# Kernel optimization log

Hardware: AMD Instinct MI355X
Metric: run time of the kernel (lower is better)

The kernel has to match this reference:

```python
import jax, jax.numpy as jnp
import numpy as np

V, D, L, H, S, MLP = 50257, 1024, 4, 16, 2048, 4
HD = D // H
EPS = 1e-5


def setup_inputs() -> dict:
    key = jax.random.key(0)
    ks = jax.random.split(key, 16)
    s = 0.02
    inp = {
        "input_ids": jax.random.randint(ks[0], (1, S), 0, V, dtype=jnp.int64),
        "emb": jax.random.normal(ks[1], (V, D), jnp.float32) * s,
        "Wq": jax.random.normal(ks[2], (L, D, D), jnp.float32) * s,
        "Wk": jax.random.normal(ks[3], (L, D, D), jnp.float32) * s,
        "Wv": jax.random.normal(ks[4], (L, D, D), jnp.float32) * s,
        "Wo": jax.random.normal(ks[5], (L, D, D), jnp.float32) * s,
        "ln1_g": jnp.ones((L, D), jnp.float32),
        "ln1_b": jnp.zeros((L, D), jnp.float32),
        "ln2_g": jnp.ones((L, D), jnp.float32),
        "ln2_b": jnp.zeros((L, D), jnp.float32),
        "W1": jax.random.normal(ks[6], (L, D, MLP * D), jnp.float32) * s,
        "b1": jnp.zeros((L, MLP * D), jnp.float32),
        "W2": jax.random.normal(ks[7], (L, MLP * D, D), jnp.float32) * s,
        "b2": jnp.zeros((L, D), jnp.float32),
        "lnf_g": jnp.ones((D,), jnp.float32),
        "lnf_b": jnp.zeros((D,), jnp.float32),
    }
    return inp


def _layer_norm(x, g, b):
    m = jnp.mean(x, axis=-1, keepdims=True)
    v = jnp.mean(jnp.square(x - m), axis=-1, keepdims=True)
    return (x - m) * jax.lax.rsqrt(v + EPS) * g + b


def _rope_cos_sin(seq_len, dtype):
    # standard RoPE: inv_freq over pairs, rotate-half convention
    inv_freq = 1.0 / (10000.0 ** (jnp.arange(0, HD, 2, dtype=jnp.float32) / HD))
    ang = jnp.arange(seq_len, dtype=jnp.float32)[:, None] * inv_freq[None, :]  # [S, HD/2]
    ang = jnp.concatenate([ang, ang], axis=-1)  # [S, HD]
    return jnp.cos(ang).astype(dtype), jnp.sin(ang).astype(dtype)


def _rotate_half(x):
    x1, x2 = x[..., : HD // 2], x[..., HD // 2 :]
    return jnp.concatenate([-x2, x1], axis=-1)


def _gpt_forward(input_ids, emb, Wq, Wk, Wv, Wo, ln1_g, ln1_b, ln2_g, ln2_b, W1, b1, W2, b2, lnf_g, lnf_b):
    B, T = input_ids.shape
    x = emb[input_ids]  # [B, T, D]
    cos, sin = _rope_cos_sin(T, x.dtype)  # [T, HD]
    cos, sin = cos[None, None], sin[None, None]  # broadcast to [B, H, T, HD]
    mask = jnp.triu(jnp.ones((T, T), dtype=bool), k=1)
    scale = 1.0 / np.sqrt(HD)
    for l in range(L):
        h = _layer_norm(x, ln1_g[l], ln1_b[l])
        q = (h @ Wq[l]).reshape(B, T, H, HD).transpose(0, 2, 1, 3)
        k = (h @ Wk[l]).reshape(B, T, H, HD).transpose(0, 2, 1, 3)
        v = (h @ Wv[l]).reshape(B, T, H, HD).transpose(0, 2, 1, 3)
        q = q * cos + _rotate_half(q) * sin
        k = k * cos + _rotate_half(k) * sin
        scores = jnp.einsum("bhsd,bhtd->bhst", q, k) * scale  # full [B,H,T,T]
        scores = jnp.where(mask, -jnp.inf, scores)
        attn = jax.nn.softmax(scores, axis=-1)
        out = jnp.einsum("bhst,bhtd->bhsd", attn, v)
        out = out.transpose(0, 2, 1, 3).reshape(B, T, D) @ Wo[l]
        x = x + out
        h = _layer_norm(x, ln2_g[l], ln2_b[l])
        x = x + (jax.nn.gelu(h @ W1[l] + b1[l], approximate=False) @ W2[l] + b2[l])
    x = _layer_norm(x, lnf_g, lnf_b)
    logits = x @ emb.T  # tied lm_head
    return logits


def reference(input_ids, emb, Wq, Wk, Wv, Wo, ln1_g, ln1_b, ln2_g, ln2_b, W1, b1, W2, b2, lnf_g, lnf_b):
    return _gpt_forward(input_ids, emb, Wq, Wk, Wv, Wo, ln1_g, ln1_b, ln2_g, ln2_b, W1, b1, W2, b2, lnf_g, lnf_b)
```

## Files before the change

kernel.cpp:

```cpp
#include <hip/hip_runtime.h>
#include <hip/hip_bf16.h>
#include <math.h>

#define TT   2048
#define DD   1024
#define NL   4
#define NH   16
#define HDIM 64
#define VV   50257
#define DMLP 4096

typedef __bf16 bf16_t;
typedef __bf16 bf16x8 __attribute__((ext_vector_type(8)));
typedef __bf16 bf16x4 __attribute__((ext_vector_type(4)));
typedef float  f32x4  __attribute__((ext_vector_type(4)));

__device__ inline float block_reduce_sum(float v) {
    __shared__ float sbuf[4];
#pragma unroll
    for (int o = 32; o > 0; o >>= 1) v += __shfl_down(v, o, 64);
    int w = threadIdx.x >> 6, lane = threadIdx.x & 63;
    __syncthreads();
    if (lane == 0) sbuf[w] = v;
    __syncthreads();
    return sbuf[0] + sbuf[1] + sbuf[2] + sbuf[3];
}

__device__ inline float block_reduce_max(float v) {
    __shared__ float mbuf[4];
#pragma unroll
    for (int o = 32; o > 0; o >>= 1) v = fmaxf(v, __shfl_down(v, o, 64));
    int w = threadIdx.x >> 6, lane = threadIdx.x & 63;
    __syncthreads();
    if (lane == 0) mbuf[w] = v;
    __syncthreads();
    return fmaxf(fmaxf(mbuf[0], mbuf[1]), fmaxf(mbuf[2], mbuf[3]));
}

__device__ __forceinline__ void async16(const bf16_t* g, bf16_t* l) {
    __builtin_amdgcn_global_load_lds(
        (const __attribute__((address_space(1))) unsigned int*)g,
        (__attribute__((address_space(3))) unsigned int*)l,
        16, 0, 0);
}

__global__ void trans_w_kernel(const float* __restrict__ in, bf16_t* __restrict__ out,
                               int K, int N, long inStride, long outStride) {
    __shared__ float tile[32][33];
    long zin  = (long)blockIdx.z * inStride;
    long zout = (long)blockIdx.z * outStride;
    int tx = threadIdx.x, ty = threadIdx.y;
    int n = blockIdx.x * 32 + tx;
    int k0 = blockIdx.y * 32;
#pragma unroll
    for (int i = 0; i < 4; i++)
        tile[ty + i * 8][tx] = in[zin + (long)(k0 + ty + i * 8) * N + n];
    __syncthreads();
    int k = k0 + tx;
#pragma unroll
    for (int i = 0; i < 4; i++) {
        int nn = blockIdx.x * 32 + ty + i * 8;
        out[zout + (long)nn * K + k] = (bf16_t)tile[tx][ty + i * 8];
    }
}

__global__ void cvt_kernel(const float* __restrict__ in, bf16_t* __restrict__ out, long n4) {
    long i = (long)blockIdx.x * 256 + threadIdx.x;
    if (i >= n4) return;
    float4 v = *(const float4*)(in + i * 4);
    bf16x4 o;
    o[0] = (bf16_t)v.x; o[1] = (bf16_t)v.y; o[2] = (bf16_t)v.z; o[3] = (bf16_t)v.w;
    *(bf16x4*)(out + i * 4) = o;
}

__global__ void gather_kernel(const int* __restrict__ ids, const float* __restrict__ emb,
                              float* __restrict__ x) {
    int row = blockIdx.x;
    int id = ids[row];
    const float4* src = (const float4*)(emb + (long)id * DD);
    float4* dst = (float4*)(x + (long)row * DD);
    dst[threadIdx.x] = src[threadIdx.x];
}

__global__ __launch_bounds__(256) void ln_kernel(const float* __restrict__ x,
                                                 const float* __restrict__ g,
                                                 const float* __restrict__ b,
                                                 bf16_t* __restrict__ out) {
    int row = blockIdx.x, tid = threadIdx.x;
    float4 v = *(const float4*)(x + (long)row * DD + tid * 4);
    float s = v.x + v.y + v.z + v.w;
    s = block_reduce_sum(s);
    float mean = s * (1.0f / DD);
    float dx = v.x - mean, dy = v.y - mean, dz = v.z - mean, dw = v.w - mean;
    float sq = dx * dx + dy * dy + dz * dz + dw * dw;
    sq = block_reduce_sum(sq);
    float inv = rsqrtf(sq * (1.0f / DD) + 1e-5f);
    float4 gv = *(const float4*)(g + tid * 4);
    float4 bv = *(const float4*)(b + tid * 4);
    bf16x4 o;
    o[0] = (bf16_t)(dx * inv * gv.x + bv.x);
    o[1] = (bf16_t)(dy * inv * gv.y + bv.y);
    o[2] = (bf16_t)(dz * inv * gv.z + bv.z);
    o[3] = (bf16_t)(dw * inv * gv.w + bv.w);
    *(bf16x4*)(out + (long)row * DD + tid * 4) = o;
}

__global__ void rope_kernel(bf16_t* __restrict__ qkv) {
    int t = blockIdx.x;
    int pIdx = blockIdx.y * 256 + threadIdx.x;
    int h = pIdx >> 5, i = pIdx & 31;
    float invf = powf(10000.0f, -(float)i * (1.0f / 32.0f));
    float ang = (float)t * invf;
    float s, c;
    sincosf(ang, &s, &c);
    long base = (long)t * 3072 + h * 64 + i;
    float q1 = (float)qkv[base], q2 = (float)qkv[base + 32];
    qkv[base]      = (bf16_t)((q1 * c - q2 * s) * 0.125f);
    qkv[base + 32] = (bf16_t)((q2 * c + q1 * s) * 0.125f);
    float k1 = (float)qkv[base + 1024], k2 = (float)qkv[base + 1056];
    qkv[base + 1024] = (bf16_t)(k1 * c - k2 * s);
    qkv[base + 1056] = (bf16_t)(k2 * c + k1 * s);
}

__global__ void trans_v_kernel(const bf16_t* __restrict__ qkv, bf16_t* __restrict__ vT) {
    __shared__ bf16_t tile[32][33];
    int t0 = blockIdx.x * 32, d0 = blockIdx.y * 32;
    int tx = threadIdx.x, ty = threadIdx.y;
#pragma unroll
    for (int i = 0; i < 4; i++)
        tile[ty + i * 8][tx] = qkv[(long)(t0 + ty + i * 8) * 3072 + 2048 + d0 + tx];
    __syncthreads();
    int t = t0 + tx;
#pragma unroll
    for (int i = 0; i < 4; i++) {
        int d = d0 + ty + i * 8;
        vT[(long)d * TT + t] = tile[tx][ty + i * 8];
    }
}

__global__ __launch_bounds__(256) void softmax_kernel(bf16_t* __restrict__ S) {
    int i = blockIdx.x, h = blockIdx.y, tid = threadIdx.x;
    bf16_t* row = S + ((long)h * TT + i) * TT;
    int len = i + 1;
    float e[8];
    float mx = -1e30f;
#pragma unroll
    for (int jj = 0; jj < 8; jj++) {
        int j = tid + jj * 256;
        e[jj] = (j < len) ? (float)row[j] : -1e30f;
        mx = fmaxf(mx, e[jj]);
    }
    mx = block_reduce_max(mx);
    float sum = 0.0f;
#pragma unroll
    for (int jj = 0; jj < 8; jj++) {
        int j = tid + jj * 256;
        if (j < len) { e[jj] = __expf(e[jj] - mx); sum += e[jj]; } else e[jj] = 0.0f;
    }
    sum = block_reduce_sum(sum);
    float inv = 1.0f / sum;
#pragma unroll
    for (int jj = 0; jj < 8; jj++)
        row[tid + jj * 256] = (bf16_t)(e[jj] * inv);
}

template <int OBF, int BIAS, int GELU, int RES>
__global__ __launch_bounds__(256, 2) void gemm_bt(
    const bf16_t* __restrict__ A, long sA, int lda,
    const bf16_t* __restrict__ Bt, long sB, int ldb,
    void* __restrict__ Cv, long sC, int ldc,
    const float* __restrict__ bias, const float* res,
    int M, int N, int K) {
    __shared__ bf16_t lA[128 * 32];
    __shared__ bf16_t lB[128 * 32];
    int bz = blockIdx.z;
    A += (long)bz * sA;
    Bt += (long)bz * sB;
    long cOff = (long)bz * sC;
    int m0 = blockIdx.x * 128, n0 = blockIdx.y * 128;
    int t = threadIdx.x;
    int wave = t >> 6, lane = t & 63;
    int wm = wave >> 1, wn = wave & 1;
    int lr = lane & 15, lq = lane >> 4;
    f32x4 acc[4][4];
#pragma unroll
    for (int a = 0; a < 4; a++)
#pragma unroll
        for (int b = 0; b < 4; b++) acc[a][b] = (f32x4){0.f, 0.f, 0.f, 0.f};

    int rowHalf = wave * 16 + (lane >> 2);
    int seg8 = (lane & 3) * 8;
    int rA0 = m0 + rowHalf;       if (rA0 > M - 1) rA0 = M - 1;
    int rA1 = m0 + rowHalf + 64;  if (rA1 > M - 1) rA1 = M - 1;
    int rB0 = n0 + rowHalf;       if (rB0 > N - 1) rB0 = N - 1;
    int rB1 = n0 + rowHalf + 64;  if (rB1 > N - 1) rB1 = N - 1;
    const bf16_t* gA0 = A + (long)rA0 * lda + seg8;
    const bf16_t* gA1 = A + (long)rA1 * lda + seg8;
    const bf16_t* gB0 = Bt + (long)rB0 * ldb + seg8;
    const bf16_t* gB1 = Bt + (long)rB1 * ldb + seg8;
    bf16_t* dA0 = lA + wave * 512;
    bf16_t* dA1 = lA + 2048 + wave * 512;
    bf16_t* dB0 = lB + wave * 512;
    bf16_t* dB1 = lB + 2048 + wave * 512;

    for (int k0 = 0; k0 < K; k0 += 32) {
        __syncthreads();
        async16(gA0 + k0, dA0);
        async16(gA1 + k0, dA1);
        async16(gB0 + k0, dB0);
        async16(gB1 + k0, dB1);
        __syncthreads();
        bf16x8 af[4], bfr[4];
#pragma unroll
        for (int mt = 0; mt < 4; mt++)
            af[mt] = *(const bf16x8*)&lA[(wm * 64 + mt * 16 + lr) * 32 + lq * 8];
#pragma unroll
        for (int nt = 0; nt < 4; nt++)
            bfr[nt] = *(const bf16x8*)&lB[(wn * 64 + nt * 16 + lr) * 32 + lq * 8];
#pragma unroll
        for (int mt = 0; mt < 4; mt++)
#pragma unroll
            for (int nt = 0; nt < 4; nt++)
                acc[mt][nt] = __builtin_amdgcn_mfma_f32_16x16x32_bf16(af[mt], bfr[nt], acc[mt][nt], 0, 0, 0);
    }
#pragma unroll
    for (int nt = 0; nt < 4; nt++) {
        int col = n0 + wn * 64 + nt * 16 + lr;
        if (col >= N) continue;
        float bb = BIAS ? bias[col] : 0.0f;
#pragma unroll
        for (int mt = 0; mt < 4; mt++) {
            int rbase = m0 + wm * 64 + mt * 16 + lq * 4;
#pragma unroll
            for (int r = 0; r < 4; r++) {
                int rowi = rbase + r;
                if (rowi >= M) continue;
                float val = acc[mt][nt][r] + bb;
                if (GELU) val = 0.5f * val * (1.0f + erff(val * 0.70710678118f));
                if (RES) val += res[(long)rowi * ldc + col];
                long idx = cOff + (long)rowi * ldc + col;
                if (OBF) ((bf16_t*)Cv)[idx] = (bf16_t)val;
                else     ((float*)Cv)[idx] = val;
            }
        }
    }
}

extern "C" void kernel_launch(void* const* d_in, const int* in_sizes, int n_in,
                              void* d_out, int out_size, void* d_ws, size_t ws_size,
                              hipStream_t stream) {
    (void)in_sizes; (void)n_in; (void)out_size; (void)ws_size;
    const int*   ids  = (const int*)d_in[0];
    const float* emb  = (const float*)d_in[1];
    const float* Wq   = (const float*)d_in[2];
    const float* Wk   = (const float*)d_in[3];
    const float* Wv   = (const float*)d_in[4];
    const float* Wo   = (const float*)d_in[5];
    const float* ln1g = (const float*)d_in[6];
    const float* ln1b = (const float*)d_in[7];
    const float* ln2g = (const float*)d_in[8];
    const float* ln2b = (const float*)d_in[9];
    const float* W1   = (const float*)d_in[10];
    const float* b1   = (const float*)d_in[11];
    const float* W2   = (const float*)d_in[12];
    const float* b2   = (const float*)d_in[13];
    const float* lnfg = (const float*)d_in[14];
    const float* lnfb = (const float*)d_in[15];
    float* out = (float*)d_out;

    char* p = (char*)d_ws;
    size_t off = 0;
    auto alloc = [&](size_t bytes) -> void* {
        void* r = p + off;
        off += (bytes + 255) & ~(size_t)255;
        return r;
    };
    bf16_t* WqkvT = (bf16_t*)alloc((size_t)NL * 3072 * 1024 * 2);
    bf16_t* WoT   = (bf16_t*)alloc((size_t)NL * 1024 * 1024 * 2);
    bf16_t* W1T   = (bf16_t*)alloc((size_t)NL * 4096 * 1024 * 2);
    bf16_t* W2T   = (bf16_t*)alloc((size_t)NL * 1024 * 4096 * 2);
    bf16_t* embB  = (bf16_t*)alloc((size_t)VV * DD * 2);
    float*  x     = (float*)alloc((size_t)TT * DD * 4);
    bf16_t* hB    = (bf16_t*)alloc((size_t)TT * DD * 2);
    bf16_t* qkv   = (bf16_t*)alloc((size_t)TT * 3072 * 2);
    bf16_t* vT    = (bf16_t*)alloc((size_t)DD * TT * 2);
    bf16_t* S     = (bf16_t*)alloc((size_t)NH * TT * TT * 2);
    bf16_t* attn  = (bf16_t*)alloc((size_t)TT * DD * 2);
    bf16_t* mlp   = (bf16_t*)alloc((size_t)TT * DMLP * 2);

    dim3 tb(32, 8);
    trans_w_kernel<<<dim3(32, 32, NL), tb, 0, stream>>>(Wq, WqkvT,                      1024, 1024, (long)1024 * 1024, (long)3072 * 1024);
    trans_w_kernel<<<dim3(32, 32, NL), tb, 0, stream>>>(Wk, WqkvT + (long)1024 * 1024,  1024, 1024, (long)1024 * 1024, (long)3072 * 1024);
    trans_w_kernel<<<dim3(32, 32, NL), tb, 0, stream>>>(Wv, WqkvT + (long)2048 * 1024,  1024, 1024, (long)1024 * 1024, (long)3072 * 1024);
    trans_w_kernel<<<dim3(32, 32, NL), tb, 0, stream>>>(Wo, WoT, 1024, 1024, (long)1024 * 1024, (long)1024 * 1024);
    trans_w_kernel<<<dim3(128, 32, NL), tb, 0, stream>>>(W1, W1T, 1024, 4096, (long)1024 * 4096, (long)4096 * 1024);
    trans_w_kernel<<<dim3(32, 128, NL), tb, 0, stream>>>(W2, W2T, 4096, 1024, (long)4096 * 1024, (long)1024 * 4096);

    long n4 = (long)VV * DD / 4;
    cvt_kernel<<<dim3((unsigned)((n4 + 255) / 256)), 256, 0, stream>>>(emb, embB, n4);
    gather_kernel<<<dim3(TT), 256, 0, stream>>>(ids, emb, x);

    for (int l = 0; l < NL; l++) {
        ln_kernel<<<TT, 256, 0, stream>>>(x, ln1g + l * DD, ln1b + l * DD, hB);
        gemm_bt<1, 0, 0, 0><<<dim3(16, 24, 1), 256, 0, stream>>>(
            hB, 0, 1024, WqkvT + (long)l * 3072 * 1024, 0, 1024,
            qkv, 0, 3072, nullptr, nullptr, 2048, 3072, 1024);
        rope_kernel<<<dim3(TT, 2), 256, 0, stream>>>(qkv);
        trans_v_kernel<<<dim3(64, 32), tb, 0, stream>>>(qkv, vT);
        gemm_bt<1, 0, 0, 0><<<dim3(16, 16, NH), 256, 0, stream>>>(
            qkv, 64, 3072, qkv + 1024, 64, 3072,
            S, (long)TT * TT, TT, nullptr, nullptr, 2048, 2048, 64);
        softmax_kernel<<<dim3(TT, NH), 256, 0, stream>>>(S);
        gemm_bt<1, 0, 0, 0><<<dim3(16, 1, NH), 256, 0, stream>>>(
            S, (long)TT * TT, TT, vT, (long)HDIM * TT, TT,
            attn, HDIM, 1024, nullptr, nullptr, 2048, HDIM, 2048);
        gemm_bt<0, 0, 0, 1><<<dim3(16, 8, 1), 256, 0, stream>>>(
            attn, 0, 1024, WoT + (long)l * 1024 * 1024, 0, 1024,
            x, 0, 1024, nullptr, x, 2048, 1024, 1024);
        ln_kernel<<<TT, 256, 0, stream>>>(x, ln2g + l * DD, ln2b + l * DD, hB);
        gemm_bt<1, 1, 1, 0><<<dim3(16, 32, 1), 256, 0, stream>>>(
            hB, 0, 1024, W1T + (long)l * 4096 * 1024, 0, 1024,
            mlp, 0, DMLP, b1 + (long)l * DMLP, nullptr, 2048, DMLP, 1024);
        gemm_bt<0, 1, 0, 1><<<dim3(16, 8, 1), 256, 0, stream>>>(
            mlp, 0, DMLP, W2T + (long)l * 1024 * 4096, 0, DMLP,
            x, 0, 1024, b2 + (long)l * DD, x, 2048, 1024, DMLP);
    }
    ln_kernel<<<TT, 256, 0, stream>>>(x, lnfg, lnfb, hB);
    gemm_bt<0, 0, 0, 0><<<dim3(16, (VV + 127) / 128, 1), 256, 0, stream>>>(
        hB, 0, 1024, embB, 0, 1024,
        out, 0, VV, nullptr, nullptr, 2048, VV, 1024);
}
```

Before: 2.518 ms.

## Replace materialized attention scores with fused causal flash-attention kernel

Replaces the QK^T GEMM, the row softmax and the PV GEMM with one flash-attention kernel. It keeps an online softmax in registers and runs MFMA on 64-row query tiles, skipping key tiles above the causal diagonal. This removes writing and re-reading the 16x2048x2048 bf16 score matrix and about half the attention FLOPs, which the old path spent on masked entries. In exchange it launches only 512 blocks and does no double buffering of K/V loads, so it may be latency-bound and the blocks are unevenly loaded.

After: 2.241 ms. 1.12x faster.

```diff
diff --git a/kernel.cpp b/kernel.cpp
--- a/kernel.cpp
+++ b/kernel.cpp
@@ -24,17 +24,6 @@
     if (lane == 0) sbuf[w] = v;
     __syncthreads();
     return sbuf[0] + sbuf[1] + sbuf[2] + sbuf[3];
-}
-
-__device__ inline float block_reduce_max(float v) {
-    __shared__ float mbuf[4];
-#pragma unroll
-    for (int o = 32; o > 0; o >>= 1) v = fmaxf(v, __shfl_down(v, o, 64));
-    int w = threadIdx.x >> 6, lane = threadIdx.x & 63;
-    __syncthreads();
-    if (lane == 0) mbuf[w] = v;
-    __syncthreads();
-    return fmaxf(fmaxf(mbuf[0], mbuf[1]), fmaxf(mbuf[2], mbuf[3]));
 }
 
 __device__ __forceinline__ void async16(const bf16_t* g, bf16_t* l) {
@@ -138,30 +127,116 @@
     }
 }
 
-__global__ __launch_bounds__(256) void softmax_kernel(bf16_t* __restrict__ S) {
-    int i = blockIdx.x, h = blockIdx.y, tid = threadIdx.x;
-    bf16_t* row = S + ((long)h * TT + i) * TT;
-    int len = i + 1;
-    float e[8];
-    float mx = -1e30f;
-#pragma unroll
-    for (int jj = 0; jj < 8; jj++) {
-        int j = tid + jj * 256;
-        e[jj] = (j < len) ? (float)row[j] : -1e30f;
-        mx = fmaxf(mx, e[jj]);
-    }
-    mx = block_reduce_max(mx);
-    float sum = 0.0f;
-#pragma unroll
-    for (int jj = 0; jj < 8; jj++) {
-        int j = tid + jj * 256;
-        if (j < len) { e[jj] = __expf(e[jj] - mx); sum += e[jj]; } else e[jj] = 0.0f;
-    }
-    sum = block_reduce_sum(sum);
-    float inv = 1.0f / sum;
-#pragma unroll
-    for (int jj = 0; jj < 8; jj++)
-        row[tid + jj * 256] = (bf16_t)(e[jj] * inv);
+__global__ __launch_bounds__(256) void flash_kernel(const bf16_t* __restrict__ qkv,
+                                                    const bf16_t* __restrict__ vT,
+                                                    bf16_t* __restrict__ attn) {
+    __shared__ bf16_t lK[4096];
+    __shared__ bf16_t lV[4096];
+    __shared__ bf16_t lP[4096];
+    int qt = 31 - blockIdx.x;
+    int h  = blockIdx.y;
+    int t  = threadIdx.x;
+    int w = t >> 6, lane = t & 63;
+    int lr = lane & 15, lq = lane >> 4;
+    int q0 = qt * 64;
+
+    const bf16_t* qrow = qkv + (long)(q0 + w * 16 + lr) * 3072 + h * 64;
+    bf16x8 qf0 = *(const bf16x8*)(qrow + lq * 8);
+    bf16x8 qf1 = *(const bf16x8*)(qrow + 32 + lq * 8);
+
+    const bf16_t* gK = qkv + 1024 + h * 64 + (long)lane * 3072;
+    const bf16_t* gV = vT + (long)(h * 64 + lane) * 2048;
+
+    bf16_t* dK0 = lK + w * 512;
+    bf16_t* dK1 = lK + w * 512 + 2048;
+    bf16_t* dV0 = lV + w * 512;
+    bf16_t* dV1 = lV + w * 512 + 2048;
+    bf16_t* wP  = lP + w * 1024;
+
+    f32x4 o[4];
+    float m[4], l[4];
+#pragma unroll
+    for (int i = 0; i < 4; i++) { o[i] = (f32x4){0.f, 0.f, 0.f, 0.f}; m[i] = -1e30f; l[i] = 0.f; }
+
+    for (int st = 0; st <= qt; st++) {
+        long kv = (long)st * 64;
+        __syncthreads();
+        async16(gK + kv * 3072 + w * 8, dK0);
+        async16(gK + kv * 3072 + (w + 4) * 8, dK1);
+        async16(gV + kv + w * 8, dV0);
+        async16(gV + kv + (w + 4) * 8, dV1);
+        __syncthreads();
+
+        f32x4 s[4];
+#pragma unroll
+        for (int nt = 0; nt < 4; nt++) {
+            s[nt] = (f32x4){0.f, 0.f, 0.f, 0.f};
+            bf16x8 kb0 = *(const bf16x8*)&lK[lq * 512 + (nt * 16 + lr) * 8];
+            bf16x8 kb1 = *(const bf16x8*)&lK[(4 + lq) * 512 + (nt * 16 + lr) * 8];
+            s[nt] = __builtin_amdgcn_mfma_f32_16x16x32_bf16(qf0, kb0, s[nt], 0, 0, 0);
+            s[nt] = __builtin_amdgcn_mfma_f32_16x16x32_bf16(qf1, kb1, s[nt], 0, 0, 0);
+        }
+        if (st == qt) {
+#pragma unroll
+            for (int nt = 0; nt < 4; nt++)
+#pragma unroll
+                for (int r = 0; r < 4; r++)
+                    if (nt * 16 + lr > w * 16 + lq * 4 + r) s[nt][r] = -1e30f;
+        }
+        float pm[4];
+#pragma unroll
+        for (int r = 0; r < 4; r++)
+            pm[r] = fmaxf(fmaxf(s[0][r], s[1][r]), fmaxf(s[2][r], s[3][r]));
+#pragma unroll
+        for (int msk = 8; msk >= 1; msk >>= 1)
+#pragma unroll
+            for (int r = 0; r < 4; r++)
+                pm[r] = fmaxf(pm[r], __shfl_xor(pm[r], msk));
+        float f[4];
+#pragma unroll
+        for (int r = 0; r < 4; r++) {
+            float nm = fmaxf(m[r], pm[r]);
+            f[r] = __expf(m[r] - nm);
+            m[r] = nm;
+        }
+        float ps[4] = {0.f, 0.f, 0.f, 0.f};
+#pragma unroll
+        for (int nt = 0; nt < 4; nt++)
+#pragma unroll
+            for (int r = 0; r < 4; r++) {
+                float p = __expf(s[nt][r] - m[r]);
+                ps[r] += p;
+                wP[((nt * 16 + lr) >> 3) * 128 + (lq * 4 + r) * 8 + (lr & 7)] = (bf16_t)p;
+            }
+#pragma unroll
+        for (int msk = 8; msk >= 1; msk >>= 1)
+#pragma unroll
+            for (int r = 0; r < 4; r++)
+                ps[r] += __shfl_xor(ps[r], msk);
+#pragma unroll
+        for (int r = 0; r < 4; r++) l[r] = l[r] * f[r] + ps[r];
+#pragma unroll
+        for (int nt = 0; nt < 4; nt++)
+#pragma unroll
+            for (int r = 0; r < 4; r++) o[nt][r] *= f[r];
+        bf16x8 pa0 = *(const bf16x8*)&wP[lq * 128 + lr * 8];
+        bf16x8 pa1 = *(const bf16x8*)&wP[(4 + lq) * 128 + lr * 8];
+#pragma unroll
+        for (int nt = 0; nt < 4; nt++) {
+            bf16x8 vb0 = *(const bf16x8*)&lV[lq * 512 + (nt * 16 + lr) * 8];
+            bf16x8 vb1 = *(const bf16x8*)&lV[(4 + lq) * 512 + (nt * 16 + lr) * 8];
+            o[nt] = __builtin_amdgcn_mfma_f32_16x16x32_bf16(pa0, vb0, o[nt], 0, 0, 0);
+            o[nt] = __builtin_amdgcn_mfma_f32_16x16x32_bf16(pa1, vb1, o[nt], 0, 0, 0);
+        }
+    }
+#pragma unroll
+    for (int r = 0; r < 4; r++) {
+        float inv = 1.0f / l[r];
+        long row = q0 + w * 16 + lq * 4 + r;
+#pragma unroll
+        for (int nt = 0; nt < 4; nt++)
+            attn[row * 1024 + h * 64 + nt * 16 + lr] = (bf16_t)(o[nt][r] * inv);
+    }
 }
 
 template <int OBF, int BIAS, int GELU, int RES>
@@ -284,7 +359,6 @@
     bf16_t* hB    = (bf16_t*)alloc((size_t)TT * DD * 2);
     bf16_t* qkv   = (bf16_t*)alloc((size_t)TT * 3072 * 2);
     bf16_t* vT    = (bf16_t*)alloc((size_t)DD * TT * 2);
-    bf16_t* S     = (bf16_t*)alloc((size_t)NH * TT * TT * 2);
     bf16_t* attn  = (bf16_t*)alloc((size_t)TT * DD * 2);
     bf16_t* mlp   = (bf16_t*)alloc((size_t)TT * DMLP * 2);
 
@@ -307,13 +381,7 @@
             qkv, 0, 3072, nullptr, nullptr, 2048, 3072, 1024);
         rope_kernel<<<dim3(TT, 2), 256, 0, stream>>>(qkv);
         trans_v_kernel<<<dim3(64, 32), tb, 0, stream>>>(qkv, vT);
-        gemm_bt<1, 0, 0, 0><<<dim3(16, 16, NH), 256, 0, stream>>>(
-            qkv, 64, 3072, qkv + 1024, 64, 3072,
-            S, (long)TT * TT, TT, nullptr, nullptr, 2048, 2048, 64);
-        softmax_kernel<<<dim3(TT, NH), 256, 0, stream>>>(S);
-        gemm_bt<1, 0, 0, 0><<<dim3(16, 1, NH), 256, 0, stream>>>(
-            S, (long)TT * TT, TT, vT, (long)HDIM * TT, TT,
-            attn, HDIM, 1024, nullptr, nullptr, 2048, HDIM, 2048);
+        flash_kernel<<<dim3(32, NH), 256, 0, stream>>>(qkv, vT, attn);
         gemm_bt<0, 0, 0, 1><<<dim3(16, 8, 1), 256, 0, stream>>>(
             attn, 0, 1024, WoT + (long)l * 1024 * 1024, 0, 1024,
             x, 0, 1024, nullptr, x, 2048, 1024, 1024);
```
